# Kernel tuning notes

Hardware: AMD Instinct MI355X
Metric: run time of the kernel (lower is better)

## Reference

```python
import jax, jax.numpy as jnp
import numpy as np

B, NQ, NK = 16, 4096, 77
QUERY_DIM, CONTEXT_DIM = 512, 768
HEADS, D_HEAD = 8, 64
INNER = HEADS * D_HEAD  # 512
SCALE = D_HEAD ** -0.5


def setup_inputs() -> dict:
    key = jax.random.key(0)
    ks = jax.random.split(key, 7)
    x = jax.random.normal(ks[0], (B, NQ, QUERY_DIM), dtype=jnp.float32)
    context = jax.random.normal(ks[1], (B, NK, CONTEXT_DIM), dtype=jnp.float32)
    # Linear weights stored as [in, out] (x @ W), matching nn.Linear math W^T.
    Wq = jax.random.normal(ks[2], (QUERY_DIM, INNER), dtype=jnp.float32) / np.sqrt(QUERY_DIM)
    Wk = jax.random.normal(ks[3], (CONTEXT_DIM, INNER), dtype=jnp.float32) / np.sqrt(CONTEXT_DIM)
    Wv = jax.random.normal(ks[4], (CONTEXT_DIM, INNER), dtype=jnp.float32) / np.sqrt(CONTEXT_DIM)
    Wo = jax.random.normal(ks[5], (INNER, QUERY_DIM), dtype=jnp.float32) / np.sqrt(INNER)
    bo = jax.random.normal(ks[6], (QUERY_DIM,), dtype=jnp.float32) * 0.02
    return {"x": x, "context": context, "Wq": Wq, "Wk": Wk, "Wv": Wv, "Wo": Wo, "bo": bo}


def reference(x, context, Wq, Wk, Wv, Wo, bo):
    b, nq, _ = x.shape
    nk = context.shape[1]
    # projections (no bias for q/k/v, as in the module)
    q = (x @ Wq).reshape(b, nq, HEADS, D_HEAD).transpose(0, 2, 1, 3)       # b h nq d
    k = (context @ Wk).reshape(b, nk, HEADS, D_HEAD).transpose(0, 2, 1, 3)  # b h nk d
    v = (context @ Wv).reshape(b, nk, HEADS, D_HEAD).transpose(0, 2, 1, 3)  # b h nk d
    # softmax(QK^T * scale) V  -- same math as the chunked torch loop
    sim = jnp.einsum('bhid,bhjd->bhij', q, k) * SCALE                       # b h nq nk
    attn = jax.nn.softmax(sim, axis=-1)
    out = jnp.einsum('bhij,bhjd->bhid', attn, v)                            # b h nq d
    out = out.transpose(0, 2, 1, 3).reshape(b, nq, INNER)                   # b nq (h d)
    return out @ Wo + bo
```

## Files before the change

kernel.cpp:

```cpp
#include <hip/hip_runtime.h>
#include <hip/hip_bf16.h>
#include <stdint.h>


typedef __attribute__((ext_vector_type(8))) short bf16x8;
typedef __attribute__((ext_vector_type(4))) float f32x4;
typedef __attribute__((ext_vector_type(4))) short short4v;
typedef __attribute__((ext_vector_type(4))) float float4v;
typedef __attribute__((ext_vector_type(2))) unsigned uint2v;
typedef __attribute__((ext_vector_type(4))) unsigned uint4v;

#define DEVINL __device__ __forceinline__

DEVINL short f2bf(float f) {
  unsigned u = __builtin_bit_cast(unsigned, f);
  unsigned r = (u + 0x7FFFu + ((u >> 16) & 1u)) >> 16;
  return (short)(unsigned short)r;
}

DEVINL unsigned pkbf(float lo, float hi) {
  unsigned r;
  asm("v_cvt_pk_bf16_f32 %0, %1, %2" : "=v"(r) : "v"(lo), "v"(hi));
  return r;
}

#define GLDS16(gp, sp)                                                \
  __builtin_amdgcn_global_load_lds(                                   \
      (const __attribute__((address_space(1))) void*)(gp),            \
      (__attribute__((address_space(3))) void*)(sp), 16, 0, 0)

__global__ __launch_bounds__(256) void prep_all(
    const float* __restrict__ Wq, const float* __restrict__ Wk,
    const float* __restrict__ Wv, const float* __restrict__ Wo,
    short* __restrict__ wqt, short* __restrict__ wkt,
    short* __restrict__ wvt, short* __restrict__ wot,
    float4v* __restrict__ vfill) {
  const int z = blockIdx.z;
  if (z == 4) {
    for (int i = (blockIdx.y * 8 + blockIdx.x) * 256 + threadIdx.x;
         i < 106496; i += 24576)
      vfill[i] = float4v{0.f, 0.f, 0.f, 0.f};
    return;
  }
  const float* W;
  short* Wt;
  int K;
  switch (z) {
    case 0: W = Wq; Wt = wqt; K = 512; break;
    case 1: W = Wk; Wt = wkt; K = 768; break;
    case 2: W = Wv; Wt = wvt; K = 768; break;
    default: W = Wo; Wt = wot; K = 512; break;
  }
  const int kt = blockIdx.y * 64;
  if (kt >= K) return;
  const int nt = blockIdx.x * 64;

  __shared__ short Tl[64][65];
#pragma unroll
  for (int i = 0; i < 16; ++i) {
    int idx = threadIdx.x + i * 256;
    int r = idx >> 6, c = idx & 63;
    Tl[c][r] = f2bf(W[(size_t)(kt + r) * 512 + nt + c]);
  }
  __syncthreads();
#pragma unroll
  for (int i = 0; i < 16; ++i) {
    int idx = threadIdx.x + i * 256;
    int r = idx >> 6, c = idx & 63;
    Wt[(size_t)(nt + r) * K + kt + c] = Tl[r][c];
  }
}

__global__ __launch_bounds__(256) void kvproj(const float* __restrict__ A,
                                              const short* __restrict__ wkt,
                                              const short* __restrict__ wvt,
                                              short* __restrict__ Kb,
                                              short* __restrict__ Vtg) {
  __shared__ short Al[32][40];
  __shared__ short Bl[128][40];

  const int TRANS = blockIdx.z;
  const short* Bt = TRANS ? wvt : wkt;

  const int tid = threadIdx.x;
  const int lane = tid & 63, wid = tid >> 6;
  const int wm = wid >> 1, wn = wid & 1;
  const int quad = lane >> 4, l16 = lane & 15;
  const int m0 = blockIdx.y * 32, n0 = blockIdx.x * 128;
  const int M = 1232, K = 768;

  f32x4 acc[4] = {};

  for (int k0 = 0; k0 < K; k0 += 32) {
    for (int idx = tid; idx < 32 * 8; idx += 256) {
      int row = idx >> 3, kq = idx & 7;
      float4v v = {};
      if (m0 + row < M)
        v = *(const float4v*)(A + (size_t)(m0 + row) * K + k0 + kq * 4);
      short4v s = {f2bf(v[0]), f2bf(v[1]), f2bf(v[2]), f2bf(v[3])};
      *(short4v*)&Al[row][kq * 4] = s;
    }
    for (int idx = tid; idx < 512; idx += 256) {
      int row = idx >> 2, kq = idx & 3;
      *(bf16x8*)&Bl[row][kq * 8] =
          *(const bf16x8*)(Bt + (size_t)(n0 + row) * K + k0 + kq * 8);
    }
    __syncthreads();

    bf16x8 a = *(bf16x8*)&Al[wm * 16 + l16][quad * 8];
#pragma unroll
    for (int n = 0; n < 4; ++n) {
      bf16x8 b = *(bf16x8*)&Bl[wn * 64 + n * 16 + l16][quad * 8];
      acc[n] = __builtin_amdgcn_mfma_f32_16x16x32_bf16(a, b, acc[n], 0, 0, 0);
    }
    __syncthreads();
  }

#pragma unroll
  for (int n = 0; n < 4; ++n) {
    const int col = n0 + wn * 64 + n * 16 + l16;
    const int rowb = m0 + wm * 16 + quad * 4;
#pragma unroll
    for (int r = 0; r < 4; ++r) {
      const int rr = rowb + r;
      if (rr < M) {
        if (!TRANS) {
          Kb[(size_t)rr * 512 + col] = f2bf(acc[n][r]);
        } else {
          const int bb = rr / 77, key = rr - bb * 77;
          Vtg[(size_t)((bb * 8 + (col >> 6)) * 64 + (col & 63)) * 104 + key] =
              f2bf(acc[n][r]);
        }
      }
    }
  }
}

__global__ __launch_bounds__(1024, 4) void qattn(const float* __restrict__ x,
                                                 const short* __restrict__ wqt,
                                                 const short* __restrict__ Kb,
                                                 const short* __restrict__ Vtg,
                                                 short* __restrict__ AOb) {
  __shared__ __align__(16) char smem[127488];
  short* xb  = (short*)smem;
  short* wsW = (short*)(smem + 20480);
  short* Qh  = (short*)smem;
  short* Kl  = (short*)(smem + 36864);
  short* Vt  = (short*)(smem + 59904);
  short* Pw  = (short*)(smem + 86528);

  const int tid = threadIdx.x;
  const int lane = tid & 63, w = tid >> 6;
  const int wm = w >> 3, wn = w & 7;
  const int quad = lane >> 4, l16 = lane & 15;
  const int m0 = blockIdx.x * 128;
  const int b = m0 >> 12;

  f32x4 acc[4][4] = {};

  const int xrow = tid >> 3, xcol = (tid & 7) * 4;
  const int wr0 = tid >> 2, wc0 = (tid & 3) * 8;
  const int wr1 = (tid + 1024) >> 2, wc1 = wc0;

  const float* xg = x + (size_t)(m0 + xrow) * 512 + xcol;
  const short* wg0 = wqt + (size_t)wr0 * 512 + wc0;
  const short* wg1 = wqt + (size_t)wr1 * 512 + wc1;

  float4v px;
  bf16x8 pw0, pw1;
  px = *(const float4v*)(xg);
  pw0 = *(const bf16x8*)(wg0);
  pw1 = *(const bf16x8*)(wg1);

  for (int t = 0; t < 16; ++t) {
    short* xbuf = xb + (t & 1) * 5120;
    short* wbuf = wsW + (t & 1) * 20480;

    *(uint2v*)&xbuf[xrow * 40 + xcol] =
        uint2v{pkbf(px[0], px[1]), pkbf(px[2], px[3])};
    *(bf16x8*)&wbuf[wr0 * 40 + wc0] = pw0;
    *(bf16x8*)&wbuf[wr1 * 40 + wc1] = pw1;

    __syncthreads();

    if (t < 15) {
      const int k1 = (t + 1) * 32;
      px = *(const float4v*)(xg + k1);
      pw0 = *(const bf16x8*)(wg0 + k1);
      pw1 = *(const bf16x8*)(wg1 + k1);
    }

    bf16x8 af[4], bfr[4];
#pragma unroll
    for (int m = 0; m < 4; ++m)
      af[m] = *(bf16x8*)&xbuf[(wm * 64 + m * 16 + l16) * 40 + quad * 8];
#pragma unroll
    for (int n = 0; n < 4; ++n)
      bfr[n] = *(bf16x8*)&wbuf[(wn * 64 + n * 16 + l16) * 40 + quad * 8];
#pragma unroll
    for (int m = 0; m < 4; ++m)
#pragma unroll
      for (int n = 0; n < 4; ++n)
        acc[m][n] = __builtin_amdgcn_mfma_f32_16x16x32_bf16(af[m], bfr[n],
                                                            acc[m][n], 0, 0, 0);
  }
  __syncthreads();

#pragma unroll
  for (int it = 0; it < 4; ++it) {
    if (it) __syncthreads();

    if ((wn >> 1) == it) {
      const int slot = wn & 1;
#pragma unroll
      for (int m = 0; m < 4; ++m)
#pragma unroll
        for (int n = 0; n < 4; ++n)
#pragma unroll
          for (int r = 0; r < 4; ++r)
            Qh[slot * 9216 + (wm * 64 + m * 16 + quad * 4 + r) * 72 +
               n * 16 + l16] = f2bf(acc[m][n][r]);
    }
    for (int idx = tid; idx < 1232; idx += 1024) {
      const int sk = idx >= 616;
      const int e = idx - sk * 616;
      const int r = e >> 3, cc = (e & 7) * 8;
      *(bf16x8*)&Kl[sk * 5760 + r * 72 + cc] =
          *(const bf16x8*)(Kb + ((size_t)b * 77 + r) * 512 +
                           (it * 2 + sk) * 64 + cc);
    }
    for (int cid = w; cid < 26; cid += 16) {
      const int sv = cid >= 13;
      const int c13 = cid - sv * 13;
      GLDS16(Vtg + (size_t)(b * 8 + it * 2 + sv) * 6656 + c13 * 512 + lane * 8,
             Vt + sv * 6656 + c13 * 512);
    }
    __syncthreads();

    bf16x8 qfr[2];
#pragma unroll
    for (int ks = 0; ks < 2; ++ks)
      qfr[ks] = *(bf16x8*)&Qh[wm * 9216 + (wn * 16 + l16) * 72 +
                              ks * 32 + quad * 8];

    f32x4 c[5] = {};
#pragma unroll
    for (int f = 0; f < 5; ++f)
#pragma unroll
      for (int ks = 0; ks < 2; ++ks) {
        bf16x8 a = *(bf16x8*)&Kl[wm * 5760 + (f * 16 + l16) * 72 +
                                 ks * 32 + quad * 8];
        c[f] = __builtin_amdgcn_mfma_f32_16x16x32_bf16(a, qfr[ks], c[f], 0, 0, 0);
      }

    float mx = -1e30f;
#pragma unroll
    for (int f = 0; f < 5; ++f)
#pragma unroll
      for (int r = 0; r < 4; ++r) {
        const int key = f * 16 + quad * 4 + r;
        float v = c[f][r] * 0.125f;
        v = (key < 77) ? v : -1e30f;
        c[f][r] = v;
        mx = fmaxf(mx, v);
      }
    mx = fmaxf(mx, __shfl_xor(mx, 16));
    mx = fmaxf(mx, __shfl_xor(mx, 32));

    short* pbase = Pw + (w * 16 + l16) * 80;
    float sum = 0.f;
#pragma unroll
    for (int f = 0; f < 5; ++f) {
      float e0 = __expf(c[f][0] - mx), e1 = __expf(c[f][1] - mx);
      float e2 = __expf(c[f][2] - mx), e3 = __expf(c[f][3] - mx);
      sum += (e0 + e1) + (e2 + e3);
      uint2v sv2 = {pkbf(e0, e1), pkbf(e2, e3)};
      *(uint2v*)(pbase + f * 16 + quad * 4) = sv2;
    }
    sum += __shfl_xor(sum, 16);
    sum += __shfl_xor(sum, 32);
    const float inv = 1.0f / sum;

    bf16x8 pb0 = *(bf16x8*)(pbase + quad * 8);
    bf16x8 pb1 = *(bf16x8*)(pbase + 32 + quad * 8);
    bf16x8 pb2 = bf16x8{0, 0, 0, 0, 0, 0, 0, 0};
    if (quad < 2) pb2 = *(bf16x8*)(pbase + 64 + quad * 8);

    f32x4 o[4] = {};
#pragma unroll
    for (int mt = 0; mt < 4; ++mt) {
      const short* vrow = &Vt[wm * 6656 + (mt * 16 + l16) * 104];
      o[mt] = __builtin_amdgcn_mfma_f32_16x16x32_bf16(
          *(bf16x8*)(vrow + quad * 8), pb0, o[mt], 0, 0, 0);
      o[mt] = __builtin_amdgcn_mfma_f32_16x16x32_bf16(
          *(bf16x8*)(vrow + 32 + quad * 8), pb1, o[mt], 0, 0, 0);
      o[mt] = __builtin_amdgcn_mfma_f32_16x16x32_bf16(
          *(bf16x8*)(vrow + 64 + quad * 8), pb2, o[mt], 0, 0, 0);
    }

    short* op = AOb + ((size_t)m0 + wn * 16 + l16) * 512 + (it * 2 + wm) * 64;
#pragma unroll
    for (int mt = 0; mt < 4; ++mt) {
      uint2v sv2 = {pkbf(o[mt][0] * inv, o[mt][1] * inv),
                    pkbf(o[mt][2] * inv, o[mt][3] * inv)};
      *(uint2v*)(op + mt * 16 + quad * 4) = sv2;
    }
  }
}

__global__ __launch_bounds__(256) void gemm2(const short* __restrict__ A,
                                             const short* __restrict__ Bt,
                                             float* __restrict__ C,
                                             const float* __restrict__ bias) {
  __shared__ short As[2][128 * 32];
  __shared__ short Bs[2][128 * 32];

  const int tid = threadIdx.x;
  const int lane = tid & 63, w = tid >> 6;
  const int wm = w >> 1, wn = w & 1;
  const int quad = lane >> 4, l16 = lane & 15;

  const int cpx = gridDim.x >> 3;
  const int swz = (blockIdx.x & 7) * cpx + (blockIdx.x >> 3);
  const int m0 = (swz >> 2) * 128, n0 = (swz & 3) * 128;

  const int lr = lane >> 2, lc = (lane & 3) * 8;

  f32x4 acc[4][4] = {};

#pragma unroll
  for (int p = 0; p < 2; ++p) {
    const int rowb = (w * 2 + p) * 16;
    GLDS16(A + (size_t)(m0 + rowb + lr) * 512 + lc, &As[0][rowb * 32]);
    GLDS16(Bt + (size_t)(n0 + rowb + lr) * 512 + lc, &Bs[0][rowb * 32]);
  }
  __syncthreads();

  for (int t = 0; t < 16; ++t) {
    const int cur = t & 1;
    if (t < 15) {
      const int k1 = (t + 1) * 32;
#pragma unroll
      for (int p = 0; p < 2; ++p) {
        const int rowb = (w * 2 + p) * 16;
        GLDS16(A + (size_t)(m0 + rowb + lr) * 512 + k1 + lc,
               &As[cur ^ 1][rowb * 32]);
        GLDS16(Bt + (size_t)(n0 + rowb + lr) * 512 + k1 + lc,
               &Bs[cur ^ 1][rowb * 32]);
      }
    }
    bf16x8 af[4], bfr[4];
#pragma unroll
    for (int m = 0; m < 4; ++m)
      af[m] = *(bf16x8*)&As[cur][(wm * 64 + m * 16 + l16) * 32 + quad * 8];
#pragma unroll
    for (int n = 0; n < 4; ++n)
      bfr[n] = *(bf16x8*)&Bs[cur][(wn * 64 + n * 16 + l16) * 32 + quad * 8];
#pragma unroll
    for (int m = 0; m < 4; ++m)
#pragma unroll
      for (int n = 0; n < 4; ++n)
        acc[m][n] = __builtin_amdgcn_mfma_f32_16x16x32_bf16(af[m], bfr[n],
                                                            acc[m][n], 0, 0, 0);
    if (t < 15) __syncthreads();
  }

#pragma unroll
  for (int m = 0; m < 4; ++m)
#pragma unroll
    for (int n = 0; n < 4; ++n) {
      const int col = n0 + wn * 64 + n * 16 + l16;
      const int rowb = m0 + wm * 64 + m * 16 + quad * 4;
      const float badd = bias[col];
#pragma unroll
      for (int r = 0; r < 4; ++r)
        C[(size_t)(rowb + r) * 512 + col] = acc[m][n][r] + badd;
    }
}

extern "C" void kernel_launch(void* const* d_in, const int* in_sizes, int n_in,
                              void* d_out, int out_size, void* d_ws, size_t ws_size,
                              hipStream_t stream) {
  const float* x   = (const float*)d_in[0];
  const float* ctx = (const float*)d_in[1];
  const float* Wq  = (const float*)d_in[2];
  const float* Wk  = (const float*)d_in[3];
  const float* Wv  = (const float*)d_in[4];
  const float* Wo  = (const float*)d_in[5];
  const float* bo  = (const float*)d_in[6];
  float* out = (float*)d_out;

  char* ws = (char*)d_ws;
  size_t off = 0;
  short* wqt = (short*)(ws + off); off += 512 * 512 * 2;
  short* wkt = (short*)(ws + off); off += 768 * 512 * 2;
  short* wvt = (short*)(ws + off); off += 768 * 512 * 2;
  short* wot = (short*)(ws + off); off += 512 * 512 * 2;
  short* Kb  = (short*)(ws + off); off += 1232 * 512 * 2;
  short* Vtg = (short*)(ws + off); off += (size_t)16 * 8 * 64 * 104 * 2;
  short* AOb = (short*)(ws + off); off += (size_t)65536 * 512 * 2;

  prep_all<<<dim3(8, 12, 5), 256, 0, stream>>>(Wq, Wk, Wv, Wo,
                                               wqt, wkt, wvt, wot,
                                               (float4v*)Vtg);
  kvproj<<<dim3(4, 39, 2), 256, 0, stream>>>(ctx, wkt, wvt, Kb, Vtg);

  qattn<<<512, 1024, 0, stream>>>(x, wqt, Kb, Vtg, AOb);

  gemm2<<<2048, 256, 0, stream>>>(AOb, wot, out, bo);
}
```

Baseline: 184.0 us.

## Split fused Q-projection attention blocks into two head-halves of 512 threads

The fused Q-projection + attention kernel now launches 1024 blocks of 512 threads. Each block computes 128 query rows for 4 heads (a 256-column slice of Wq) instead of 8 heads with 1024 threads. Shared memory per block is halved, which should let more blocks co-reside per CU and improve load balance across CUs. The cost is that each block still loads and converts its full x tile, so x is read and converted twice overall.

```diff
diff --git a/kernel.cpp b/kernel.cpp
--- a/kernel.cpp
+++ b/kernel.cpp
@@ -136,58 +136,61 @@
   }
 }
 
-__global__ __launch_bounds__(1024, 4) void qattn(const float* __restrict__ x,
-                                                 const short* __restrict__ wqt,
-                                                 const short* __restrict__ Kb,
-                                                 const short* __restrict__ Vtg,
-                                                 short* __restrict__ AOb) {
-  __shared__ __align__(16) char smem[127488];
+__global__ __launch_bounds__(512, 4) void qattn(const float* __restrict__ x,
+                                                const short* __restrict__ wqt,
+                                                const short* __restrict__ Kb,
+                                                const short* __restrict__ Vtg,
+                                                short* __restrict__ AOb) {
+  __shared__ __align__(16) char smem[63744];
   short* xb  = (short*)smem;
   short* wsW = (short*)(smem + 20480);
   short* Qh  = (short*)smem;
-  short* Kl  = (short*)(smem + 36864);
-  short* Vt  = (short*)(smem + 59904);
-  short* Pw  = (short*)(smem + 86528);
+  short* Kl  = (short*)(smem + 18432);
+  short* Vt  = (short*)(smem + 29952);
+  short* Pw  = (short*)(smem + 43264);
 
   const int tid = threadIdx.x;
   const int lane = tid & 63, w = tid >> 6;
-  const int wm = w >> 3, wn = w & 7;
+  const int wm = w >> 2, wn = w & 3;
   const int quad = lane >> 4, l16 = lane & 15;
-  const int m0 = blockIdx.x * 128;
-  const int b = m0 >> 12;
+  const int qt = blockIdx.x & 511, ch = blockIdx.x >> 9;
+  const int m0 = qt * 128;
+  const int b = qt >> 5;
+  const int n0 = ch * 256;
 
   f32x4 acc[4][4] = {};
 
-  const int xrow = tid >> 3, xcol = (tid & 7) * 4;
-  const int wr0 = tid >> 2, wc0 = (tid & 3) * 8;
-  const int wr1 = (tid + 1024) >> 2, wc1 = wc0;
+  const int xrow = tid >> 2, xcol = (tid & 3) * 8;
+  const int wr = tid >> 1, wc = (tid & 1) * 16;
 
   const float* xg = x + (size_t)(m0 + xrow) * 512 + xcol;
-  const short* wg0 = wqt + (size_t)wr0 * 512 + wc0;
-  const short* wg1 = wqt + (size_t)wr1 * 512 + wc1;
-
-  float4v px;
+  const short* wg = wqt + (size_t)(n0 + wr) * 512 + wc;
+
+  float4v pxa, pxb;
   bf16x8 pw0, pw1;
-  px = *(const float4v*)(xg);
-  pw0 = *(const bf16x8*)(wg0);
-  pw1 = *(const bf16x8*)(wg1);
+  pxa = *(const float4v*)(xg);
+  pxb = *(const float4v*)(xg + 4);
+  pw0 = *(const bf16x8*)(wg);
+  pw1 = *(const bf16x8*)(wg + 8);
 
   for (int t = 0; t < 16; ++t) {
     short* xbuf = xb + (t & 1) * 5120;
-    short* wbuf = wsW + (t & 1) * 20480;
-
-    *(uint2v*)&xbuf[xrow * 40 + xcol] =
-        uint2v{pkbf(px[0], px[1]), pkbf(px[2], px[3])};
-    *(bf16x8*)&wbuf[wr0 * 40 + wc0] = pw0;
-    *(bf16x8*)&wbuf[wr1 * 40 + wc1] = pw1;
+    short* wbuf = wsW + (t & 1) * 10240;
+
+    uint4v u = {pkbf(pxa[0], pxa[1]), pkbf(pxa[2], pxa[3]),
+                pkbf(pxb[0], pxb[1]), pkbf(pxb[2], pxb[3])};
+    *(bf16x8*)&xbuf[xrow * 40 + xcol] = __builtin_bit_cast(bf16x8, u);
+    *(bf16x8*)&wbuf[wr * 40 + wc] = pw0;
+    *(bf16x8*)&wbuf[wr * 40 + wc + 8] = pw1;
 
     __syncthreads();
 
     if (t < 15) {
       const int k1 = (t + 1) * 32;
-      px = *(const float4v*)(xg + k1);
-      pw0 = *(const bf16x8*)(wg0 + k1);
-      pw1 = *(const bf16x8*)(wg1 + k1);
+      pxa = *(const float4v*)(xg + k1);
+      pxb = *(const float4v*)(xg + k1 + 4);
+      pw0 = *(const bf16x8*)(wg + k1);
+      pw1 = *(const bf16x8*)(wg + k1 + 8);
     }
 
     bf16x8 af[4], bfr[4];
@@ -209,47 +212,39 @@
 #pragma unroll
   for (int it = 0; it < 4; ++it) {
     if (it) __syncthreads();
-
-    if ((wn >> 1) == it) {
-      const int slot = wn & 1;
+    const int h = ch * 4 + it;
+
+    if (wn == it) {
 #pragma unroll
       for (int m = 0; m < 4; ++m)
 #pragma unroll
         for (int n = 0; n < 4; ++n)
 #pragma unroll
           for (int r = 0; r < 4; ++r)
-            Qh[slot * 9216 + (wm * 64 + m * 16 + quad * 4 + r) * 72 +
-               n * 16 + l16] = f2bf(acc[m][n][r]);
-    }
-    for (int idx = tid; idx < 1232; idx += 1024) {
-      const int sk = idx >= 616;
-      const int e = idx - sk * 616;
-      const int r = e >> 3, cc = (e & 7) * 8;
-      *(bf16x8*)&Kl[sk * 5760 + r * 72 + cc] =
-          *(const bf16x8*)(Kb + ((size_t)b * 77 + r) * 512 +
-                           (it * 2 + sk) * 64 + cc);
-    }
-    for (int cid = w; cid < 26; cid += 16) {
-      const int sv = cid >= 13;
-      const int c13 = cid - sv * 13;
-      GLDS16(Vtg + (size_t)(b * 8 + it * 2 + sv) * 6656 + c13 * 512 + lane * 8,
-             Vt + sv * 6656 + c13 * 512);
-    }
+            Qh[(wm * 64 + m * 16 + quad * 4 + r) * 72 + n * 16 + l16] =
+                f2bf(acc[m][n][r]);
+    }
+    for (int idx = tid; idx < 616; idx += 512) {
+      const int r = idx >> 3, cc = (idx & 7) * 8;
+      *(bf16x8*)&Kl[r * 72 + cc] =
+          *(const bf16x8*)(Kb + ((size_t)b * 77 + r) * 512 + h * 64 + cc);
+    }
+    for (int cid = w; cid < 13; cid += 8)
+      GLDS16(Vtg + (size_t)(b * 8 + h) * 6656 + cid * 512 + lane * 8,
+             Vt + cid * 512);
     __syncthreads();
 
     bf16x8 qfr[2];
 #pragma unroll
     for (int ks = 0; ks < 2; ++ks)
-      qfr[ks] = *(bf16x8*)&Qh[wm * 9216 + (wn * 16 + l16) * 72 +
-                              ks * 32 + quad * 8];
+      qfr[ks] = *(bf16x8*)&Qh[(w * 16 + l16) * 72 + ks * 32 + quad * 8];
 
     f32x4 c[5] = {};
 #pragma unroll
     for (int f = 0; f < 5; ++f)
 #pragma unroll
       for (int ks = 0; ks < 2; ++ks) {
-        bf16x8 a = *(bf16x8*)&Kl[wm * 5760 + (f * 16 + l16) * 72 +
-                                 ks * 32 + quad * 8];
+        bf16x8 a = *(bf16x8*)&Kl[(f * 16 + l16) * 72 + ks * 32 + quad * 8];
         c[f] = __builtin_amdgcn_mfma_f32_16x16x32_bf16(a, qfr[ks], c[f], 0, 0, 0);
       }
 
@@ -289,7 +284,7 @@
     f32x4 o[4] = {};
 #pragma unroll
     for (int mt = 0; mt < 4; ++mt) {
-      const short* vrow = &Vt[wm * 6656 + (mt * 16 + l16) * 104];
+      const short* vrow = &Vt[(mt * 16 + l16) * 104];
       o[mt] = __builtin_amdgcn_mfma_f32_16x16x32_bf16(
           *(bf16x8*)(vrow + quad * 8), pb0, o[mt], 0, 0, 0);
       o[mt] = __builtin_amdgcn_mfma_f32_16x16x32_bf16(
@@ -298,7 +293,7 @@
           *(bf16x8*)(vrow + 64 + quad * 8), pb2, o[mt], 0, 0, 0);
     }
 
-    short* op = AOb + ((size_t)m0 + wn * 16 + l16) * 512 + (it * 2 + wm) * 64;
+    short* op = AOb + ((size_t)m0 + w * 16 + l16) * 512 + h * 64;
 #pragma unroll
     for (int mt = 0; mt < 4; ++mt) {
       uint2v sv2 = {pkbf(o[mt][0] * inv, o[mt][1] * inv),
@@ -405,7 +400,7 @@
                                                (float4v*)Vtg);
   kvproj<<<dim3(4, 39, 2), 256, 0, stream>>>(ctx, wkt, wvt, Kb, Vtg);
 
-  qattn<<<512, 1024, 0, stream>>>(x, wqt, Kb, Vtg, AOb);
+  qattn<<<1024, 512, 0, stream>>>(x, wqt, Kb, Vtg, AOb);
 
   gemm2<<<2048, 256, 0, stream>>>(AOb, wot, out, bo);
 }
```

New measurement: 179.9 us. 1.02x faster.
